# Kernel optimization log

Measured on AMD Instinct MI355X. Metric: run time of the kernel, lower is better.

The kernel has to match this reference:

```python
import jax, jax.numpy as jnp
import numpy as np

B, H, W, C = 2, 128, 128, 128
NS = 8                      # attn_num_splits
WH, WW = H // NS, W // NS   # window size 16x16
SH, SW = WH // 2, WW // 2   # shift sizes
HID = 2 * C * 4             # ffn hidden (in_channels = 2*d_model, expansion 4)
EPS = 1e-5


def _make_swin_mask():
    # Standard shifted-window attention mask: -100 between different regions.
    img = np.zeros((H, W), np.int32)
    cnt = 0
    for hs in (slice(0, -WH), slice(-WH, -SH), slice(-SH, None)):
        for ws in (slice(0, -WW), slice(-WW, -SW), slice(-SW, None)):
            img[hs, ws] = cnt
            cnt += 1
    ids = img.reshape(NS, WH, NS, WW).transpose(0, 2, 1, 3).reshape(NS * NS, WH * WW)
    mask = np.where(ids[:, None, :] != ids[:, :, None], -100.0, 0.0).astype(np.float32)
    return jnp.asarray(mask)  # (64, 256, 256)


def _layernorm(x, g, b):
    m = jnp.mean(x, axis=-1, keepdims=True)
    v = jnp.mean(jnp.square(x - m), axis=-1, keepdims=True)
    return (x - m) * jax.lax.rsqrt(v + EPS) * g + b


def setup_inputs() -> dict:
    key = jax.random.key(0)
    ks = jax.random.split(key, 8)
    s = 1.0 / np.sqrt(C)
    return {
        "source": jax.random.normal(ks[0], (B, H * W, C), jnp.float32),
        "target": jax.random.normal(ks[1], (B, H * W, C), jnp.float32),
        "Wq": jax.random.normal(ks[2], (C, C), jnp.float32) * s,
        "Wk": jax.random.normal(ks[3], (C, C), jnp.float32) * s,
        "Wv": jax.random.normal(ks[4], (C, C), jnp.float32) * s,
        "Wm": jax.random.normal(ks[5], (C, C), jnp.float32) * s,
        "g1": jnp.ones((C,), jnp.float32),
        "b1": jnp.zeros((C,), jnp.float32),
        "W1": jax.random.normal(ks[6], (2 * C, HID), jnp.float32) * (1.0 / np.sqrt(2 * C)),
        "W2": jax.random.normal(ks[7], (HID, C), jnp.float32) * (1.0 / np.sqrt(HID)),
        "g2": jnp.ones((C,), jnp.float32),
        "b2": jnp.zeros((C,), jnp.float32),
        "shifted_window_attn_mask": _make_swin_mask(),
        "height": H,
        "width": W,
        "attn_num_splits": NS,
    }


def reference(source, target, Wq, Wk, Wv, Wm, g1, b1, W1, W2, g2, b2,
              shifted_window_attn_mask, height, width, attn_num_splits):
    b, L, c = source.shape
    h, w, ns = height, width, attn_num_splits
    wh, ww = h // ns, w // ns
    sh, sw = wh // 2, ww // 2

    q = source @ Wq
    k = target @ Wk
    v = target @ Wv

    def to_windows(x):
        # (b, h*w, c) -> shifted -> (b, nWin, wh*ww, c)
        x = x.reshape(b, h, w, c)
        x = jnp.roll(x, (-sh, -sw), axis=(1, 2))
        x = x.reshape(b, ns, wh, ns, ww, c).transpose(0, 1, 3, 2, 4, 5)
        return x.reshape(b, ns * ns, wh * ww, c)

    qw, kw, vw = to_windows(q), to_windows(k), to_windows(v)
    scores = jnp.einsum('bnlc,bnmc->bnlm', qw, kw) / (c ** 0.5)
    scores = scores + shifted_window_attn_mask[None]  # broadcast over batch
    attn = jax.nn.softmax(scores, axis=-1)
    out = jnp.einsum('bnlm,bnmc->bnlc', attn, vw)

    # merge windows back and undo the shift
    out = out.reshape(b, ns, ns, wh, ww, c).transpose(0, 1, 3, 2, 4, 5).reshape(b, h, w, c)
    out = jnp.roll(out, (sh, sw), axis=(1, 2)).reshape(b, h * w, c)

    message = _layernorm(out @ Wm, g1, b1)
    ffn_in = jnp.concatenate([source, message], axis=-1)
    message = jax.nn.gelu(ffn_in @ W1, approximate=False) @ W2
    message = _layernorm(message, g2, b2)
    return source + message
```

## Files before the change

### kernel.cpp

```cpp
#include <hip/hip_runtime.h>
#include <math.h>
#include <stdint.h>


typedef unsigned short u16;
typedef __attribute__((ext_vector_type(8))) short bf16x8;
typedef __attribute__((ext_vector_type(4))) float f32x4;
typedef __attribute__((ext_vector_type(16))) float f32x16;
typedef __attribute__((ext_vector_type(4))) short u16x4;

__device__ __forceinline__ u16 f2b(float f) {
    unsigned int i = __float_as_uint(f);
    unsigned int r = (i + 0x7fffu + ((i >> 16) & 1u)) >> 16;
    return (u16)r;
}

__device__ __forceinline__ float gelu_e(float x) {
    float y = fabsf(x) * 0.70710678118f;
    float u = fmaf(y, fmaf(y, fmaf(y, fmaf(y, 0.078108f, 0.000972f),
                                   0.230389f), 0.278393f), 1.0f);
    u = u * u; u = u * u;
    float r = __builtin_amdgcn_rcpf(u);
    return fmaxf(x, 0.f) - 0.5f * fabsf(x) * r;
}

__device__ __forceinline__ void cp16(const void* g, void* l) {
    auto* gp = reinterpret_cast<const __attribute__((address_space(1))) unsigned int*>(
        reinterpret_cast<uintptr_t>(g));
    auto* lp = reinterpret_cast<__attribute__((address_space(3))) unsigned int*>(
        reinterpret_cast<uintptr_t>(l));
    __builtin_amdgcn_global_load_lds(gp, lp, 16, 0, 0);
}

__device__ __forceinline__ int win_map(int gm) {
    int b = gm >> 14, rr = gm & 16383;
    int win = rr >> 8, t = rr & 255;
    int wi = win >> 3, wj = win & 7, i = t >> 4, j = t & 15;
    int h = (wi * 16 + i + 8) & 127;
    int w = (wj * 16 + j + 8) & 127;
    return (b << 14) + h * 128 + w;
}

__global__ __launch_bounds__(256, 2)
void gemm_qkv(const u16* __restrict__ srcb, const u16* __restrict__ tgtb,
              const u16* __restrict__ Bt, u16* __restrict__ qw,
              u16* __restrict__ kw, u16* __restrict__ vwt)
{
    __shared__ __align__(16) u16 SMEM[32768];
    u16* As = SMEM;
    u16* Bs = SMEM + 16384;
    u16* Ts = SMEM;

    const int tid = threadIdx.x;
    const int w = tid >> 6, lane = tid & 63;
    const int lm = lane & 15, q = lane >> 4;
    const int wm = w >> 1, wn = w & 1;
    const int m0 = blockIdx.x * 128;
    const int y = blockIdx.y;
    const u16* Ab = (y == 0) ? srcb : tgtb;

#pragma unroll
    for (int s = 0; s < 4; ++s)
#pragma unroll
        for (int i = 0; i < 2; ++i) {
            int row = w * 32 + i * 16 + (lane >> 2);
            int kc = s * 32 + (lane & 3) * 8;
            cp16(Ab + (size_t)win_map(m0 + row) * 128 + kc,
                 (void*)(As + (s * 128 + w * 32 + i * 16) * 32));
            cp16(Bt + (size_t)(y * 128 + row) * 128 + kc,
                 (void*)(Bs + (s * 128 + w * 32 + i * 16) * 32));
        }
    __syncthreads();

    f32x4 acc[4][4] = {};
#pragma unroll
    for (int s = 0; s < 4; ++s) {
        bf16x8 af[4], bfr[4];
#pragma unroll
        for (int t = 0; t < 4; ++t)
            af[t] = *(const bf16x8*)(As + (s * 128 + wm * 64 + t * 16 + lm) * 32 + q * 8);
#pragma unroll
        for (int t = 0; t < 4; ++t)
            bfr[t] = *(const bf16x8*)(Bs + (s * 128 + wn * 64 + t * 16 + lm) * 32 + q * 8);
#pragma unroll
        for (int mt = 0; mt < 4; ++mt)
#pragma unroll
            for (int nt = 0; nt < 4; ++nt)
                acc[mt][nt] = __builtin_amdgcn_mfma_f32_16x16x32_bf16(
                    af[mt], bfr[nt], acc[mt][nt], 0, 0, 0);
    }

    __syncthreads();
#pragma unroll
    for (int mt = 0; mt < 4; ++mt)
#pragma unroll
        for (int nt = 0; nt < 4; ++nt)
#pragma unroll
            for (int r = 0; r < 4; ++r) {
                int rowl = wm * 64 + mt * 16 + q * 4 + r;
                int col = wn * 64 + nt * 16 + lm;
                int idx = (y == 2) ? col * 136 + rowl : rowl * 136 + col;
                Ts[idx] = f2b(acc[mt][nt][r]);
            }
    __syncthreads();
    const int c8 = (tid & 15) * 8;
#pragma unroll
    for (int i = 0; i < 8; ++i) {
        int rr = i * 16 + (tid >> 4);
        bf16x8 t = *(const bf16x8*)(Ts + rr * 136 + c8);
        if (y == 2) {
            int wix = m0 >> 8, tok0 = m0 & 255;
            *(bf16x8*)(vwt + (size_t)wix * 32768 + (size_t)rr * 256 + tok0 + c8) = t;
        } else {
            u16* Cv = (y == 0) ? qw : kw;
            *(bf16x8*)(Cv + (size_t)(m0 + rr) * 128 + c8) = t;
        }
    }
}

__global__ __launch_bounds__(256, 2)
void gemm_ffn1(const u16* __restrict__ A0, const u16* __restrict__ A1,
               const u16* __restrict__ Bt, u16* __restrict__ C)
{
    __shared__ __align__(16) u16 SMEM[32768];
    u16* As = SMEM;
    u16* Bs = SMEM + 16384;

    const int tid = threadIdx.x;
    const int w = tid >> 6, lane = tid & 63;
    const int l32 = lane & 31, lh = lane >> 5;
    const int wm = w >> 1, wn = w & 1;
    const int m0 = blockIdx.x * 128, n0 = blockIdx.y * 128;

    f32x16 acc[2][2] = {};
#pragma unroll
    for (int kt2 = 0; kt2 < 2; ++kt2) {
        __syncthreads();
        const u16* Ab = kt2 ? A1 : A0;
#pragma unroll
        for (int s = 0; s < 4; ++s)
#pragma unroll
            for (int i = 0; i < 2; ++i) {
                int row = w * 32 + i * 16 + (lane >> 2);
                int kc = s * 32 + (lane & 3) * 8;
                cp16(Ab + (size_t)(m0 + row) * 128 + kc,
                     (void*)(As + (s * 128 + w * 32 + i * 16) * 32));
                cp16(Bt + (size_t)(n0 + row) * 256 + kt2 * 128 + kc,
                     (void*)(Bs + (s * 128 + w * 32 + i * 16) * 32));
            }
        __syncthreads();
#pragma unroll
        for (int s = 0; s < 4; ++s)
#pragma unroll
            for (int kc = 0; kc < 2; ++kc) {
                bf16x8 af[2], bfr[2];
#pragma unroll
                for (int mt = 0; mt < 2; ++mt)
                    af[mt] = *(const bf16x8*)(As + (s * 128 + wm * 64 + mt * 32 + l32) * 32
                                              + kc * 16 + lh * 8);
#pragma unroll
                for (int nt = 0; nt < 2; ++nt)
                    bfr[nt] = *(const bf16x8*)(Bs + (s * 128 + wn * 64 + nt * 32 + l32) * 32
                                               + kc * 16 + lh * 8);
#pragma unroll
                for (int mt = 0; mt < 2; ++mt)
#pragma unroll
                    for (int nt = 0; nt < 2; ++nt)
                        acc[mt][nt] = __builtin_amdgcn_mfma_f32_32x32x16_bf16(
                            af[mt], bfr[nt], acc[mt][nt], 0, 0, 0);
            }
    }

#pragma unroll
    for (int mt = 0; mt < 2; ++mt)
#pragma unroll
        for (int nt = 0; nt < 2; ++nt) {
            int col = n0 + wn * 64 + nt * 32 + l32;
            int rbase = m0 + wm * 64 + mt * 32 + 4 * lh;
#pragma unroll
            for (int r = 0; r < 16; ++r) {
                int row = rbase + (r & 3) + 8 * (r >> 2);
                C[(size_t)row * 1024 + col] = f2b(gelu_e(acc[mt][nt][r]));
            }
        }
}

__global__ __launch_bounds__(256)
void attn_msg(const u16* __restrict__ qw, const u16* __restrict__ kw,
              const u16* __restrict__ vt, const u16* __restrict__ wmt,
              const float* __restrict__ g, const float* __restrict__ bb,
              u16* __restrict__ msgb)
{
    __shared__ __align__(16) u16 Ps[64 * 264];

    const int tid = threadIdx.x, w = tid >> 6, lane = tid & 63;
    const int lm = lane & 15, q = lane >> 4;
    const int bid = blockIdx.x;
    const int qc = bid & 3, win = (bid >> 2) & 63, b = bid >> 8;
    const int wi = win >> 3, wj = win & 7;
    const int q0 = qc * 64;
    const size_t wbase = (size_t)(b * 64 + win);
    const u16* kwb = kw + wbase * 256 * 128;
    const u16* qwb = qw + wbase * 256 * 128;
    const u16* vtb = vt + wbase * 128 * 256;

    bf16x8 af[4];
    const u16* qrow = qwb + (size_t)(q0 + w * 16 + lm) * 128;
#pragma unroll
    for (int kt = 0; kt < 4; ++kt)
        af[kt] = *(const bf16x8*)(qrow + kt * 32 + q * 8);

    f32x4 s[16];
#pragma unroll
    for (int nt = 0; nt < 16; ++nt) { f32x4 z = {0.f, 0.f, 0.f, 0.f}; s[nt] = z; }
#pragma unroll
    for (int kt = 0; kt < 4; ++kt)
#pragma unroll
        for (int nt = 0; nt < 16; ++nt) {
            bf16x8 bf = *(const bf16x8*)(kwb + (size_t)(nt * 16 + lm) * 128 + kt * 32 + q * 8);
            s[nt] = __builtin_amdgcn_mfma_f32_16x16x32_bf16(af[kt], bf, s[nt], 0, 0, 0);
        }

    int idk[16];
#pragma unroll
    for (int nt = 0; nt < 16; ++nt) {
        int rh = (wi == 7) ? ((nt >= 8) ? 2 : 1) : 0;
        int rw = (wj == 7) ? ((lm >= 8) ? 2 : 1) : 0;
        idk[nt] = rh * 3 + rw;
    }
    const float scale = 0.08838834764831845f;
#pragma unroll
    for (int r = 0; r < 4; ++r) {
        int tq = q0 + w * 16 + q * 4 + r;
        int iq = tq >> 4, jq = tq & 15;
        int rhq = (wi == 7) ? ((iq >= 8) ? 2 : 1) : 0;
        int rwq = (wj == 7) ? ((jq >= 8) ? 2 : 1) : 0;
        int idq = rhq * 3 + rwq;
        float sv[16];
        float mx = -1e30f;
#pragma unroll
        for (int nt = 0; nt < 16; ++nt) {
            float x = s[nt][r] * scale + ((idq != idk[nt]) ? -100.f : 0.f);
            sv[nt] = x; mx = fmaxf(mx, x);
        }
        mx = fmaxf(mx, __shfl_xor(mx, 1));
        mx = fmaxf(mx, __shfl_xor(mx, 2));
        mx = fmaxf(mx, __shfl_xor(mx, 4));
        mx = fmaxf(mx, __shfl_xor(mx, 8));
        float sum = 0.f;
#pragma unroll
        for (int nt = 0; nt < 16; ++nt) { float e = __expf(sv[nt] - mx); sv[nt] = e; sum += e; }
        sum += __shfl_xor(sum, 1);
        sum += __shfl_xor(sum, 2);
        sum += __shfl_xor(sum, 4);
        sum += __shfl_xor(sum, 8);
        float inv = 1.0f / sum;
#pragma unroll
        for (int nt = 0; nt < 16; ++nt)
            Ps[(w * 16 + q * 4 + r) * 264 + nt * 16 + lm] = f2b(sv[nt] * inv);
    }
    __syncthreads();

    f32x4 o[8];
#pragma unroll
    for (int nt = 0; nt < 8; ++nt) { f32x4 z = {0.f, 0.f, 0.f, 0.f}; o[nt] = z; }
#pragma unroll
    for (int tt = 0; tt < 8; ++tt) {
        bf16x8 pf = *(const bf16x8*)(Ps + (w * 16 + lm) * 264 + tt * 32 + q * 8);
#pragma unroll
        for (int nt = 0; nt < 8; ++nt) {
            bf16x8 vf = *(const bf16x8*)(vtb + (size_t)(nt * 16 + lm) * 256 + tt * 32 + q * 8);
            o[nt] = __builtin_amdgcn_mfma_f32_16x16x32_bf16(pf, vf, o[nt], 0, 0, 0);
        }
    }

    __syncthreads();
    u16* Ot = Ps;
#pragma unroll
    for (int r = 0; r < 4; ++r) {
        int rl = w * 16 + q * 4 + r;
#pragma unroll
        for (int nt = 0; nt < 8; ++nt)
            Ot[rl * 136 + nt * 16 + lm] = f2b(o[nt][r]);
    }
    __syncthreads();

    f32x4 macc[8];
#pragma unroll
    for (int n2 = 0; n2 < 8; ++n2) { f32x4 z = {0.f, 0.f, 0.f, 0.f}; macc[n2] = z; }
#pragma unroll
    for (int kt = 0; kt < 4; ++kt) {
        bf16x8 paf = *(const bf16x8*)(Ot + (w * 16 + lm) * 136 + kt * 32 + q * 8);
#pragma unroll
        for (int n2 = 0; n2 < 8; ++n2) {
            bf16x8 wf = *(const bf16x8*)(wmt + (size_t)(n2 * 16 + lm) * 128 + kt * 32 + q * 8);
            macc[n2] = __builtin_amdgcn_mfma_f32_16x16x32_bf16(paf, wf, macc[n2], 0, 0, 0);
        }
    }

    float gv[8], bv[8];
#pragma unroll
    for (int n2 = 0; n2 < 8; ++n2) {
        int col = n2 * 16 + lm;
        gv[n2] = g[col]; bv[n2] = bb[col];
    }
#pragma unroll
    for (int r = 0; r < 4; ++r) {
        float s1 = 0.f, s2 = 0.f;
#pragma unroll
        for (int n2 = 0; n2 < 8; ++n2) {
            float v = macc[n2][r];
            s1 += v; s2 += v * v;
        }
        s1 += __shfl_xor(s1, 1); s2 += __shfl_xor(s2, 1);
        s1 += __shfl_xor(s1, 2); s2 += __shfl_xor(s2, 2);
        s1 += __shfl_xor(s1, 4); s2 += __shfl_xor(s2, 4);
        s1 += __shfl_xor(s1, 8); s2 += __shfl_xor(s2, 8);
        float mean = s1 * (1.f / 128.f);
        float var = fmaxf(s2 * (1.f / 128.f) - mean * mean, 0.f);
        float rs = rsqrtf(var + 1e-5f);
        int t = q0 + w * 16 + q * 4 + r;
        int ii = t >> 4, jj = t & 15;
        int h = (wi * 16 + ii + 8) & 127;
        int w2 = (wj * 16 + jj + 8) & 127;
        size_t orow = ((size_t)b * 16384 + h * 128 + w2) * 128;
#pragma unroll
        for (int n2 = 0; n2 < 8; ++n2)
            msgb[orow + n2 * 16 + lm] = f2b((macc[n2][r] - mean) * rs * gv[n2] + bv[n2]);
    }
}

__global__ __launch_bounds__(256, 3)
void gemm_ffn2(const u16* __restrict__ A, const u16* __restrict__ Bt,
               const float* __restrict__ g, const float* __restrict__ bb,
               const float* __restrict__ resid, float* __restrict__ outv)
{
    __shared__ __align__(16) u16 SMEM[25088];
    u16* As = SMEM;
    u16* Bs = SMEM + 8192;
    float* stats = (float*)(SMEM + 24576);

    const int tid = threadIdx.x;
    const int w = tid >> 6, lane = tid & 63;
    const int lm = lane & 15, q = lane >> 4;
    const int wm = w >> 1, wn = w & 1;
    const int m0 = blockIdx.x * 64;
    const int K = 1024;

    f32x4 acc[2][4] = {};
#pragma unroll
    for (int kt2 = 0; kt2 < 8; ++kt2) {
        __syncthreads();
#pragma unroll
        for (int s = 0; s < 4; ++s) {
            int kc = kt2 * 128 + s * 32 + (lane & 3) * 8;
            int arow = w * 16 + (lane >> 2);
            cp16(A + (size_t)(m0 + arow) * K + kc,
                 (void*)(As + (s * 64 + w * 16) * 32));
#pragma unroll
            for (int i = 0; i < 2; ++i) {
                int brow = w * 32 + i * 16 + (lane >> 2);
                cp16(Bt + (size_t)brow * K + kc,
                     (void*)(Bs + (s * 128 + w * 32 + i * 16) * 32));
            }
        }
        __syncthreads();
#pragma unroll
        for (int s = 0; s < 4; ++s) {
            bf16x8 af[2], bfr[4];
#pragma unroll
            for (int t = 0; t < 2; ++t)
                af[t] = *(const bf16x8*)(As + (s * 64 + wm * 32 + t * 16 + lm) * 32 + q * 8);
#pragma unroll
            for (int t = 0; t < 4; ++t)
                bfr[t] = *(const bf16x8*)(Bs + (s * 128 + wn * 64 + t * 16 + lm) * 32 + q * 8);
#pragma unroll
            for (int mt = 0; mt < 2; ++mt)
#pragma unroll
                for (int nt = 0; nt < 4; ++nt)
                    acc[mt][nt] = __builtin_amdgcn_mfma_f32_16x16x32_bf16(
                        af[mt], bfr[nt], acc[mt][nt], 0, 0, 0);
        }
    }

#pragma unroll
    for (int mt = 0; mt < 2; ++mt)
#pragma unroll
        for (int r = 0; r < 4; ++r) {
            float s1 = 0.f, s2 = 0.f;
#pragma unroll
            for (int nt = 0; nt < 4; ++nt) {
                float v = acc[mt][nt][r];
                s1 += v; s2 += v * v;
            }
            s1 += __shfl_xor(s1, 1); s2 += __shfl_xor(s2, 1);
            s1 += __shfl_xor(s1, 2); s2 += __shfl_xor(s2, 2);
            s1 += __shfl_xor(s1, 4); s2 += __shfl_xor(s2, 4);
            s1 += __shfl_xor(s1, 8); s2 += __shfl_xor(s2, 8);
            if (lm == 0) {
                int row = wm * 32 + mt * 16 + q * 4 + r;
                stats[row * 4 + wn * 2] = s1;
                stats[row * 4 + wn * 2 + 1] = s2;
            }
        }
    __syncthreads();

    float gv[4], bv[4];
#pragma unroll
    for (int nt = 0; nt < 4; ++nt) {
        int col = wn * 64 + nt * 16 + lm;
        gv[nt] = g[col]; bv[nt] = bb[col];
    }
#pragma unroll
    for (int mt = 0; mt < 2; ++mt)
#pragma unroll
        for (int r = 0; r < 4; ++r) {
            int row = wm * 32 + mt * 16 + q * 4 + r;
            f32x4 st = *(const f32x4*)(stats + row * 4);
            float mean = (st[0] + st[2]) * (1.f / 128.f);
            float var = fmaxf((st[1] + st[3]) * (1.f / 128.f) - mean * mean, 0.f);
            float rs = rsqrtf(var + 1e-5f);
#pragma unroll
            for (int nt = 0; nt < 4; ++nt) {
                int col = wn * 64 + nt * 16 + lm;
                size_t gi = (size_t)(m0 + row) * 128 + col;
                outv[gi] = (acc[mt][nt][r] - mean) * rs * gv[nt] + bv[nt] + resid[gi];
            }
        }
}

__global__ void prep_all(const float* __restrict__ Wq, const float* __restrict__ Wk,
                         const float* __restrict__ Wv, const float* __restrict__ Wm,
                         const float* __restrict__ W1, const float* __restrict__ W2,
                         const float* __restrict__ src, const float* __restrict__ tgt,
                         u16* __restrict__ ws, u16* __restrict__ srcb,
                         u16* __restrict__ tgtb)
{
    int bx = blockIdx.x;
    if (bx < 1792) {
        int idx = bx * 256 + threadIdx.x;
        if (idx < 65536) {
            int m = idx >> 14, e = idx & 16383;
            const float* sp = (m == 0) ? Wq : (m == 1) ? Wk : (m == 2) ? Wv : Wm;
            int n = e >> 7, k = e & 127;
            ws[m * 16384 + n * 128 + k] = f2b(sp[k * 128 + n]);
        } else if (idx < 327680) {
            int e = idx - 65536;
            int n = e >> 8, k = e & 255;
            ws[65536 + n * 256 + k] = f2b(W1[k * 1024 + n]);
        } else {
            int e = idx - 327680;
            int n = e >> 10, k = e & 1023;
            ws[327680 + n * 1024 + k] = f2b(W2[k * 128 + n]);
        }
    } else {
        int idx = (bx - 1792) * 256 + threadIdx.x;
        const float* s; u16* d; int i;
        if (idx < 1048576) { s = src; d = srcb; i = idx * 4; }
        else               { s = tgt; d = tgtb; i = (idx - 1048576) * 4; }
        f32x4 v = *(const f32x4*)(s + i);
        u16x4 o; o[0] = f2b(v[0]); o[1] = f2b(v[1]); o[2] = f2b(v[2]); o[3] = f2b(v[3]);
        *(u16x4*)(d + i) = o;
    }
}

#define OFF_WQT  0u
#define OFF_WMT  49152u
#define OFF_W1T  65536u
#define OFF_W2T  327680u
#define OFF_SRCB 458752u
#define OFF_TGTB 4653056u
#define OFF_QW   8847360u
#define OFF_KW   13041664u
#define OFF_VWT  17235968u
#define OFF_MSGB 21430272u
#define OFF_HID  25624576u

extern "C" void kernel_launch(void* const* d_in, const int* in_sizes, int n_in,
                              void* d_out, int out_size, void* d_ws, size_t ws_size,
                              hipStream_t stream)
{
    (void)in_sizes; (void)n_in; (void)out_size; (void)ws_size;
    const float* source = (const float*)d_in[0];
    const float* target = (const float*)d_in[1];
    const float* Wq = (const float*)d_in[2];
    const float* Wk = (const float*)d_in[3];
    const float* Wv = (const float*)d_in[4];
    const float* Wm = (const float*)d_in[5];
    const float* g1 = (const float*)d_in[6];
    const float* b1 = (const float*)d_in[7];
    const float* W1 = (const float*)d_in[8];
    const float* W2 = (const float*)d_in[9];
    const float* g2 = (const float*)d_in[10];
    const float* b2 = (const float*)d_in[11];
    u16* ws = (u16*)d_ws;
    float* out = (float*)d_out;

    prep_all<<<9984, 256, 0, stream>>>(Wq, Wk, Wv, Wm, W1, W2, source, target,
                                       ws, ws + OFF_SRCB, ws + OFF_TGTB);
    gemm_qkv<<<dim3(256, 3), 256, 0, stream>>>(
        ws + OFF_SRCB, ws + OFF_TGTB, ws + OFF_WQT,
        ws + OFF_QW, ws + OFF_KW, ws + OFF_VWT);
    attn_msg<<<512, 256, 0, stream>>>(
        ws + OFF_QW, ws + OFF_KW, ws + OFF_VWT, ws + OFF_WMT, g1, b1,
        ws + OFF_MSGB);
    gemm_ffn1<<<dim3(256, 8), 256, 0, stream>>>(
        ws + OFF_SRCB, ws + OFF_MSGB, ws + OFF_W1T, ws + OFF_HID);
    gemm_ffn2<<<512, 256, 0, stream>>>(
        ws + OFF_HID, ws + OFF_W2T, g2, b2, source, out);
}
```

Measured before the change: 232.5 us.

## Stage Q, K, V and Wm tiles through shared memory in attention kernel

The attention+message kernel now copies Q, K (in two halves), V^T (in two halves) and the Wm weights into an LDS buffer with 16-byte async-style copies, and the MFMA operand fragments are read from LDS instead of scattered global loads. This turns many strided global reads into coalesced bulk copies. It also sets launch bounds to request two blocks per CU. In exchange it adds a 32KB LDS buffer and several extra block barriers, which may limit occupancy and serialize copies with compute.

```diff
diff --git a/kernel.cpp b/kernel.cpp
--- a/kernel.cpp
+++ b/kernel.cpp
@@ -185,16 +185,18 @@
         }
 }
 
-__global__ __launch_bounds__(256)
+__global__ __launch_bounds__(256, 2)
 void attn_msg(const u16* __restrict__ qw, const u16* __restrict__ kw,
               const u16* __restrict__ vt, const u16* __restrict__ wmt,
               const float* __restrict__ g, const float* __restrict__ bb,
               u16* __restrict__ msgb)
 {
     __shared__ __align__(16) u16 Ps[64 * 264];
+    __shared__ __align__(16) u16 B32[16384];
 
     const int tid = threadIdx.x, w = tid >> 6, lane = tid & 63;
     const int lm = lane & 15, q = lane >> 4;
+    const int l4r = lane >> 2, l4c = (lane & 3) * 8;
     const int bid = blockIdx.x;
     const int qc = bid & 3, win = (bid >> 2) & 63, b = bid >> 8;
     const int wi = win >> 3, wj = win & 7;
@@ -204,11 +206,25 @@
     const u16* qwb = qw + wbase * 256 * 128;
     const u16* vtb = vt + wbase * 128 * 256;
 
+    u16* Qs = Ps;
+#pragma unroll
+    for (int i = 0; i < 4; ++i)
+        cp16(qwb + (size_t)(q0 + w * 16 + l4r) * 128 + i * 32 + l4c,
+             (void*)(Qs + (i * 64 + w * 16) * 32));
+#pragma unroll
+    for (int s = 0; s < 4; ++s)
+#pragma unroll
+        for (int i = 0; i < 2; ++i) {
+            int tok = w * 32 + i * 16 + l4r;
+            cp16(kwb + (size_t)tok * 128 + s * 32 + l4c,
+                 (void*)(B32 + (s * 128 + w * 32 + i * 16) * 32));
+        }
+    __syncthreads();
+
     bf16x8 af[4];
-    const u16* qrow = qwb + (size_t)(q0 + w * 16 + lm) * 128;
 #pragma unroll
     for (int kt = 0; kt < 4; ++kt)
-        af[kt] = *(const bf16x8*)(qrow + kt * 32 + q * 8);
+        af[kt] = *(const bf16x8*)(Qs + (kt * 64 + w * 16 + lm) * 32 + q * 8);
 
     f32x4 s[16];
 #pragma unroll
@@ -216,9 +232,36 @@
 #pragma unroll
     for (int kt = 0; kt < 4; ++kt)
 #pragma unroll
-        for (int nt = 0; nt < 16; ++nt) {
-            bf16x8 bf = *(const bf16x8*)(kwb + (size_t)(nt * 16 + lm) * 128 + kt * 32 + q * 8);
+        for (int nt = 0; nt < 8; ++nt) {
+            bf16x8 bf = *(const bf16x8*)(B32 + (kt * 128 + nt * 16 + lm) * 32 + q * 8);
             s[nt] = __builtin_amdgcn_mfma_f32_16x16x32_bf16(af[kt], bf, s[nt], 0, 0, 0);
+        }
+    __syncthreads();
+#pragma unroll
+    for (int ss = 0; ss < 4; ++ss)
+#pragma unroll
+        for (int i = 0; i < 2; ++i) {
+            int tok = 128 + w * 32 + i * 16 + l4r;
+            cp16(kwb + (size_t)tok * 128 + ss * 32 + l4c,
+                 (void*)(B32 + (ss * 128 + w * 32 + i * 16) * 32));
+        }
+    __syncthreads();
+#pragma unroll
+    for (int kt = 0; kt < 4; ++kt)
+#pragma unroll
+        for (int nt = 8; nt < 16; ++nt) {
+            bf16x8 bf = *(const bf16x8*)(B32 + (kt * 128 + (nt - 8) * 16 + lm) * 32 + q * 8);
+            s[nt] = __builtin_amdgcn_mfma_f32_16x16x32_bf16(af[kt], bf, s[nt], 0, 0, 0);
+        }
+    __syncthreads();
+
+#pragma unroll
+    for (int tt = 0; tt < 4; ++tt)
+#pragma unroll
+        for (int i = 0; i < 2; ++i) {
+            int ch = w * 32 + i * 16 + l4r;
+            cp16(vtb + (size_t)ch * 256 + tt * 32 + l4c,
+                 (void*)(B32 + (tt * 128 + w * 32 + i * 16) * 32));
         }
 
     int idk[16];
@@ -265,16 +308,43 @@
 #pragma unroll
     for (int nt = 0; nt < 8; ++nt) { f32x4 z = {0.f, 0.f, 0.f, 0.f}; o[nt] = z; }
 #pragma unroll
-    for (int tt = 0; tt < 8; ++tt) {
+    for (int tt = 0; tt < 4; ++tt) {
         bf16x8 pf = *(const bf16x8*)(Ps + (w * 16 + lm) * 264 + tt * 32 + q * 8);
 #pragma unroll
         for (int nt = 0; nt < 8; ++nt) {
-            bf16x8 vf = *(const bf16x8*)(vtb + (size_t)(nt * 16 + lm) * 256 + tt * 32 + q * 8);
+            bf16x8 vf = *(const bf16x8*)(B32 + (tt * 128 + nt * 16 + lm) * 32 + q * 8);
             o[nt] = __builtin_amdgcn_mfma_f32_16x16x32_bf16(pf, vf, o[nt], 0, 0, 0);
         }
     }
-
-    __syncthreads();
+    __syncthreads();
+#pragma unroll
+    for (int tt = 0; tt < 4; ++tt)
+#pragma unroll
+        for (int i = 0; i < 2; ++i) {
+            int ch = w * 32 + i * 16 + l4r;
+            cp16(vtb + (size_t)ch * 256 + 128 + tt * 32 + l4c,
+                 (void*)(B32 + (tt * 128 + w * 32 + i * 16) * 32));
+        }
+    __syncthreads();
+#pragma unroll
+    for (int tt = 4; tt < 8; ++tt) {
+        bf16x8 pf = *(const bf16x8*)(Ps + (w * 16 + lm) * 264 + tt * 32 + q * 8);
+#pragma unroll
+        for (int nt = 0; nt < 8; ++nt) {
+            bf16x8 vf = *(const bf16x8*)(B32 + ((tt - 4) * 128 + nt * 16 + lm) * 32 + q * 8);
+            o[nt] = __builtin_amdgcn_mfma_f32_16x16x32_bf16(pf, vf, o[nt], 0, 0, 0);
+        }
+    }
+    __syncthreads();
+
+#pragma unroll
+    for (int ss = 0; ss < 4; ++ss)
+#pragma unroll
+        for (int i = 0; i < 2; ++i) {
+            int n = w * 32 + i * 16 + l4r;
+            cp16(wmt + (size_t)n * 128 + ss * 32 + l4c,
+                 (void*)(B32 + (ss * 128 + w * 32 + i * 16) * 32));
+        }
     u16* Ot = Ps;
 #pragma unroll
     for (int r = 0; r < 4; ++r) {
@@ -293,7 +363,7 @@
         bf16x8 paf = *(const bf16x8*)(Ot + (w * 16 + lm) * 136 + kt * 32 + q * 8);
 #pragma unroll
         for (int n2 = 0; n2 < 8; ++n2) {
-            bf16x8 wf = *(const bf16x8*)(wmt + (size_t)(n2 * 16 + lm) * 128 + kt * 32 + q * 8);
+            bf16x8 wf = *(const bf16x8*)(B32 + (kt * 128 + n2 * 16 + lm) * 32 + q * 8);
             macc[n2] = __builtin_amdgcn_mfma_f32_16x16x32_bf16(paf, wf, macc[n2], 0, 0, 0);
         }
     }
```

Result: faster. 207.8 us (-10.6%).
